# Performance work log

Measured on AMD Instinct MI355X. Metric: run time of the kernel, lower is better.

## Reference

```python
import jax, jax.numpy as jnp
import numpy as np

EPS = 1e-12  # torch F.normalize eps

def _l2n(x, axis):
    n = jnp.linalg.norm(x, axis=axis, keepdims=True)
    return x / jnp.maximum(n, EPS)

def setup_inputs() -> dict:
    key = jax.random.key(0)
    ks = jax.random.split(key, 11)
    B, N, D = 8, 4096, 512
    s = 1.0 / np.sqrt(D)
    return {
        'a': jax.random.normal(ks[0], (B, N, D), jnp.float32),
        'b': jax.random.normal(ks[1], (B, N, D), jnp.float32),
        'Wq': jax.random.normal(ks[2], (D, D), jnp.float32) * s,
        'bq': jax.random.normal(ks[3], (D,), jnp.float32) * s,
        'Wk': jax.random.normal(ks[4], (D, D), jnp.float32) * s,
        'bk': jax.random.normal(ks[5], (D,), jnp.float32) * s,
        'w_g': jax.random.normal(ks[6], (D, 1), jnp.float32),
        'Wp': jax.random.normal(ks[7], (D, D), jnp.float32) * s,
        'bp': jax.random.normal(ks[8], (D,), jnp.float32) * s,
        'Wf': jax.random.normal(ks[9], (D, D), jnp.float32) * s,
        'bf': jax.random.normal(ks[10], (D,), jnp.float32) * s,
    }

def reference(a, b, Wq, bq, Wk, bk, w_g, Wp, bp, Wf, bf):
    D = a.shape[-1]
    scale = D ** (-0.5)
    query = _l2n(jnp.einsum('bnd,ed->bne', a, Wq) + bq, axis=-1)   # [B,N,D]
    key = _l2n(jnp.einsum('bnd,ed->bne', b, Wk) + bk, axis=-1)     # [B,N,D]
    A = (query @ w_g) * scale                                      # [B,N,1]
    A = _l2n(A, axis=1)                                            # normalize over seq
    G = jnp.sum(A * query, axis=1)                                 # [B,D] learned pooling
    gk = G[:, None, :] * key                                       # broadcast [B,N,D]
    out = jnp.einsum('bnd,ed->bne', gk, Wp) + bp + query           # residual
    out = jnp.einsum('bnd,ed->bne', out, Wf) + bf
    return out
```

## Files before the change

### kernel.cpp

```cpp
#include <hip/hip_runtime.h>
#include <stdint.h>

#define DD 512
#define MTOT 32768

typedef float f32x4 __attribute__((ext_vector_type(4)));
typedef __bf16 bf16x8 __attribute__((ext_vector_type(8)));

__device__ __forceinline__ unsigned short f2bf(float f) {
  union { float f; unsigned int u; } c; c.f = f;
  unsigned int r = c.u + 0x7fffu + ((c.u >> 16) & 1u);
  return (unsigned short)(r >> 16);
}
__device__ __forceinline__ float bf2f(unsigned short h) {
  union { unsigned int u; float f; } c; c.u = ((unsigned int)h) << 16;
  return c.f;
}

union FragU { uint4 u; bf16x8 b; };

__global__ __launch_bounds__(256) void convw_k(const float* __restrict__ Wq,
    const float* __restrict__ Wk, const float* __restrict__ Wp,
    const float* __restrict__ Wf, unsigned short* __restrict__ out) {
  int i = (blockIdx.x * 256 + threadIdx.x) * 4;
  int slab = i >> 18;
  int off = i & 262143;
  const float* src = slab == 0 ? Wq : slab == 1 ? Wk : slab == 2 ? Wp : Wf;
  float4 f = *(const float4*)(src + off);
  ushort4 h;
  h.x = f2bf(f.x); h.y = f2bf(f.y); h.z = f2bf(f.z); h.w = f2bf(f.w);
  *(ushort4*)(out + i) = h;
}

template<int AMODE, int EMODE>
__global__ __launch_bounds__(256) void gemm_k(const void* __restrict__ Xv,
    const unsigned short* __restrict__ W, const float* __restrict__ bias,
    const float* __restrict__ Gm, const unsigned short* __restrict__ Qadd,
    void* __restrict__ Cv) {
  constexpr int BM = 128, BK = 32, LDA = 40;
  __shared__ unsigned short As[BM * LDA];
  __shared__ unsigned short Bs[BM * LDA];
  const int tid = threadIdx.x;
  const int lane = tid & 63, wave = tid >> 6;
  const int wr = (wave >> 1) * 64, wc = (wave & 1) * 64;
  const int row0 = blockIdx.x * BM;
  const int col0 = blockIdx.y * BM;
  const int srow = tid >> 1;
  const int skk = (tid & 1) * 16;
  const int fr = lane & 15, quad = lane >> 4;

  f32x4 acc[4][4] = {};

  const float* Gb = nullptr;
  if (AMODE == 2) Gb = Gm + (size_t)(row0 >> 12) * DD;

  for (int k0 = 0; k0 < DD; k0 += BK) {
    unsigned short* adst = &As[srow * LDA + skk];
    if (AMODE == 0) {
      const float* Xr = (const float*)Xv + (size_t)(row0 + srow) * DD + k0 + skk;
#pragma unroll
      for (int q = 0; q < 4; q++) {
        float4 f = ((const float4*)Xr)[q];
        ushort4 h; h.x = f2bf(f.x); h.y = f2bf(f.y); h.z = f2bf(f.z); h.w = f2bf(f.w);
        *(ushort4*)(adst + q * 4) = h;
      }
    } else if (AMODE == 1) {
      const uint4* Xr = (const uint4*)((const unsigned short*)Xv +
                                       (size_t)(row0 + srow) * DD + k0 + skk);
      *(uint4*)adst = Xr[0];
      *(uint4*)(adst + 8) = Xr[1];
    } else {
      const unsigned short* Xr = (const unsigned short*)Xv +
                                 (size_t)(row0 + srow) * DD + k0 + skk;
      const float* Gk = Gb + k0 + skk;
#pragma unroll
      for (int q = 0; q < 4; q++) {
        ushort4 x = *(const ushort4*)(Xr + q * 4);
        float4 g = ((const float4*)Gk)[q];
        ushort4 h;
        h.x = f2bf(bf2f(x.x) * g.x);
        h.y = f2bf(bf2f(x.y) * g.y);
        h.z = f2bf(bf2f(x.z) * g.z);
        h.w = f2bf(bf2f(x.w) * g.w);
        *(ushort4*)(adst + q * 4) = h;
      }
    }
    {
      const uint4* Wr = (const uint4*)(W + (size_t)(col0 + srow) * DD + k0 + skk);
      unsigned short* bdst = &Bs[srow * LDA + skk];
      *(uint4*)bdst = Wr[0];
      *(uint4*)(bdst + 8) = Wr[1];
    }
    __syncthreads();
    bf16x8 af[4], bfr[4];
#pragma unroll
    for (int i = 0; i < 4; i++) {
      FragU u; u.u = *(const uint4*)&As[(wr + i * 16 + fr) * LDA + quad * 8];
      af[i] = u.b;
    }
#pragma unroll
    for (int j = 0; j < 4; j++) {
      FragU u; u.u = *(const uint4*)&Bs[(wc + j * 16 + fr) * LDA + quad * 8];
      bfr[j] = u.b;
    }
#pragma unroll
    for (int i = 0; i < 4; i++)
#pragma unroll
      for (int j = 0; j < 4; j++)
        acc[i][j] = __builtin_amdgcn_mfma_f32_16x16x32_bf16(af[i], bfr[j], acc[i][j], 0, 0, 0);
    __syncthreads();
  }
#pragma unroll
  for (int j = 0; j < 4; j++) {
    int gc = col0 + wc + j * 16 + fr;
    float bv = bias[gc];
#pragma unroll
    for (int i = 0; i < 4; i++) {
      int gr0 = row0 + wr + i * 16 + quad * 4;
#pragma unroll
      for (int r = 0; r < 4; r++) {
        size_t idx = (size_t)(gr0 + r) * DD + gc;
        float v = acc[i][j][r] + bv;
        if (EMODE == 1) v += bf2f(Qadd[idx]);
        if (EMODE <= 1) ((unsigned short*)Cv)[idx] = f2bf(v);
        else            ((float*)Cv)[idx] = v;
      }
    }
  }
}

__global__ __launch_bounds__(256) void norm_k(unsigned short* __restrict__ Q,
    unsigned short* __restrict__ K, const float* __restrict__ wg,
    float* __restrict__ Araw) {
  const int lane = threadIdx.x & 63, wave = threadIdx.x >> 6;
  const size_t row = (size_t)blockIdx.x * 4 + wave;
  unsigned short* p = (blockIdx.y == 0 ? Q : K) + row * DD + lane * 8;
  uint4 u = *(uint4*)p;
  unsigned short* hp = (unsigned short*)&u;
  float v[8];
  float ss = 0.f;
#pragma unroll
  for (int t = 0; t < 8; t++) { v[t] = bf2f(hp[t]); ss += v[t] * v[t]; }
#pragma unroll
  for (int m = 1; m < 64; m <<= 1) ss += __shfl_xor(ss, m, 64);
  float inv = 1.0f / fmaxf(sqrtf(ss), 1e-12f);
#pragma unroll
  for (int t = 0; t < 8; t++) { v[t] *= inv; hp[t] = f2bf(v[t]); }
  *(uint4*)p = u;
  if (blockIdx.y == 0) {
    const float4* wp = (const float4*)(wg + lane * 8);
    float4 w0 = wp[0], w1 = wp[1];
    float dot = v[0] * w0.x + v[1] * w0.y + v[2] * w0.z + v[3] * w0.w +
                v[4] * w1.x + v[5] * w1.y + v[6] * w1.z + v[7] * w1.w;
#pragma unroll
    for (int m = 1; m < 64; m <<= 1) dot += __shfl_xor(dot, m, 64);
    if (lane == 0) Araw[row] = dot;
  }
}

__global__ __launch_bounds__(512) void reduce_s_k(const float* __restrict__ Araw,
    float* __restrict__ sinv, float* __restrict__ G) {
  const int b = blockIdx.x, t = threadIdx.x;
  G[b * DD + t] = 0.f;
  float ss = 0.f;
  for (int i = t; i < 4096; i += 512) { float v = Araw[b * 4096 + i]; ss += v * v; }
#pragma unroll
  for (int m = 1; m < 64; m <<= 1) ss += __shfl_xor(ss, m, 64);
  __shared__ float sred[8];
  if ((t & 63) == 0) sred[t >> 6] = ss;
  __syncthreads();
  if (t == 0) {
    float tot = 0.f;
    for (int i = 0; i < 8; i++) tot += sred[i];
    sinv[b] = 1.0f / fmaxf(sqrtf(tot), 1e-12f);
  }
}

__global__ __launch_bounds__(256) void pool_k(const float* __restrict__ Araw,
    const float* __restrict__ sinv, const unsigned short* __restrict__ Q,
    float* __restrict__ G) {
  const int b = blockIdx.x >> 5;
  const int chunk = blockIdx.x & 31;
  const int rbase = b * 4096 + chunk * 128;
  const float si = sinv[b];
  const int t = threadIdx.x;
  float a0 = 0.f, a1 = 0.f;
  for (int r = 0; r < 128; r++) {
    float w = Araw[rbase + r] * si;
    const unsigned short* qr = Q + (size_t)(rbase + r) * DD;
    a0 += w * bf2f(qr[t]);
    a1 += w * bf2f(qr[t + 256]);
  }
  atomicAdd(&G[b * DD + t], a0);
  atomicAdd(&G[b * DD + t + 256], a1);
}

extern "C" void kernel_launch(void* const* d_in, const int* in_sizes, int n_in,
                              void* d_out, int out_size, void* d_ws, size_t ws_size,
                              hipStream_t stream) {
  const float* a   = (const float*)d_in[0];
  const float* b   = (const float*)d_in[1];
  const float* Wq  = (const float*)d_in[2];
  const float* bq  = (const float*)d_in[3];
  const float* Wk  = (const float*)d_in[4];
  const float* bk  = (const float*)d_in[5];
  const float* wg  = (const float*)d_in[6];
  const float* Wp  = (const float*)d_in[7];
  const float* bp  = (const float*)d_in[8];
  const float* Wf  = (const float*)d_in[9];
  const float* bfb = (const float*)d_in[10];

  char* ws = (char*)d_ws;
  const size_t WELEM = 262144;
  const size_t MD = (size_t)MTOT * DD;
  unsigned short* Wqb = (unsigned short*)ws;
  unsigned short* Wkb = Wqb + WELEM;
  unsigned short* Wpb = Wkb + WELEM;
  unsigned short* Wfb = Wpb + WELEM;
  unsigned short* Qb  = (unsigned short*)(ws + (size_t)2097152);
  unsigned short* Kb  = Qb + MD;
  unsigned short* O1b = Kb + MD;
  float* Araw = (float*)(ws + (size_t)2097152 + 3 * MD * 2);
  float* sinv = Araw + MTOT;
  float* G    = sinv + 64;

  convw_k<<<dim3(1024), dim3(256), 0, stream>>>(Wq, Wk, Wp, Wf, Wqb);
  gemm_k<0, 0><<<dim3(MTOT / 128, 4), dim3(256), 0, stream>>>(a, Wqb, bq, nullptr, nullptr, Qb);
  gemm_k<0, 0><<<dim3(MTOT / 128, 4), dim3(256), 0, stream>>>(b, Wkb, bk, nullptr, nullptr, Kb);
  norm_k<<<dim3(MTOT / 4, 2), dim3(256), 0, stream>>>(Qb, Kb, wg, Araw);
  reduce_s_k<<<dim3(8), dim3(512), 0, stream>>>(Araw, sinv, G);
  pool_k<<<dim3(256), dim3(256), 0, stream>>>(Araw, sinv, Qb, G);
  gemm_k<2, 1><<<dim3(MTOT / 128, 4), dim3(256), 0, stream>>>(Kb, Wpb, bp, G, Qb, O1b);
  gemm_k<1, 2><<<dim3(MTOT / 128, 4), dim3(256), 0, stream>>>(O1b, Wfb, bfb, nullptr, nullptr, d_out);
}
```

Measured before the change: 358.6 us.

## Use direct global-to-LDS loads with swizzled BK=64 tiles and fold G into weights

```diff
diff --git a/kernel.cpp b/kernel.cpp
--- a/kernel.cpp
+++ b/kernel.cpp
@@ -7,107 +7,115 @@
 typedef float f32x4 __attribute__((ext_vector_type(4)));
 typedef __bf16 bf16x8 __attribute__((ext_vector_type(8)));
 
-__device__ __forceinline__ unsigned short f2bf(float f) {
+static __device__ __forceinline__ unsigned short f2bf(float f) {
   union { float f; unsigned int u; } c; c.f = f;
   unsigned int r = c.u + 0x7fffu + ((c.u >> 16) & 1u);
   return (unsigned short)(r >> 16);
 }
-__device__ __forceinline__ float bf2f(unsigned short h) {
+static __device__ __forceinline__ float bf2f(unsigned short h) {
   union { unsigned int u; float f; } c; c.u = ((unsigned int)h) << 16;
   return c.f;
 }
 
 union FragU { uint4 u; bf16x8 b; };
 
-__global__ __launch_bounds__(256) void convw_k(const float* __restrict__ Wq,
-    const float* __restrict__ Wk, const float* __restrict__ Wp,
-    const float* __restrict__ Wf, unsigned short* __restrict__ out) {
+static __device__ __forceinline__ void load_lds16(const void* g, void* l) {
+  __builtin_amdgcn_global_load_lds(
+      (const __attribute__((address_space(1))) void*)g,
+      (__attribute__((address_space(3))) void*)l, 16, 0, 0);
+}
+
+__global__ __launch_bounds__(256) void cvt_k(const float* __restrict__ src,
+                                             unsigned short* __restrict__ dst) {
   int i = (blockIdx.x * 256 + threadIdx.x) * 4;
-  int slab = i >> 18;
-  int off = i & 262143;
-  const float* src = slab == 0 ? Wq : slab == 1 ? Wk : slab == 2 ? Wp : Wf;
-  float4 f = *(const float4*)(src + off);
+  float4 f = *(const float4*)(src + i);
   ushort4 h;
   h.x = f2bf(f.x); h.y = f2bf(f.y); h.z = f2bf(f.z); h.w = f2bf(f.w);
+  *(ushort4*)(dst + i) = h;
+}
+
+__global__ __launch_bounds__(256) void cvt3w_k(const float* __restrict__ W0,
+    const float* __restrict__ W1, const float* __restrict__ W2,
+    unsigned short* __restrict__ D0, unsigned short* __restrict__ D1,
+    unsigned short* __restrict__ D2) {
+  int slab = blockIdx.x >> 8;
+  int off = ((blockIdx.x & 255) * 256 + threadIdx.x) * 4;
+  const float* s = slab == 0 ? W0 : slab == 1 ? W1 : W2;
+  unsigned short* d = slab == 0 ? D0 : slab == 1 ? D1 : D2;
+  float4 f = *(const float4*)(s + off);
+  ushort4 h;
+  h.x = f2bf(f.x); h.y = f2bf(f.y); h.z = f2bf(f.z); h.w = f2bf(f.w);
+  *(ushort4*)(d + off) = h;
+}
+
+__global__ __launch_bounds__(256) void scalew_k(const float* __restrict__ Wp,
+    const float* __restrict__ G, unsigned short* __restrict__ out) {
+  int i = (blockIdx.x * 256 + threadIdx.x) * 4;
+  int b = i >> 18;
+  int rem = i & 262143;
+  int d = rem & 511;
+  float4 w = *(const float4*)(Wp + rem);
+  float4 g = *(const float4*)(G + b * DD + d);
+  ushort4 h;
+  h.x = f2bf(w.x * g.x); h.y = f2bf(w.y * g.y);
+  h.z = f2bf(w.z * g.z); h.w = f2bf(w.w * g.w);
   *(ushort4*)(out + i) = h;
 }
 
-template<int AMODE, int EMODE>
-__global__ __launch_bounds__(256) void gemm_k(const void* __restrict__ Xv,
-    const unsigned short* __restrict__ W, const float* __restrict__ bias,
-    const float* __restrict__ Gm, const unsigned short* __restrict__ Qadd,
+template<int BBATCH, int EMODE>
+__global__ __launch_bounds__(256) void gemm_k(
+    const unsigned short* __restrict__ X,
+    const unsigned short* __restrict__ Wb,
+    const float* __restrict__ bias,
+    const unsigned short* __restrict__ Qadd,
     void* __restrict__ Cv) {
-  constexpr int BM = 128, BK = 32, LDA = 40;
-  __shared__ unsigned short As[BM * LDA];
-  __shared__ unsigned short Bs[BM * LDA];
+  __shared__ unsigned short As[128 * 64];
+  __shared__ unsigned short Bs[128 * 64];
   const int tid = threadIdx.x;
   const int lane = tid & 63, wave = tid >> 6;
+  const int row0 = blockIdx.x * 128, col0 = blockIdx.y * 128;
+  const unsigned short* W = Wb + (BBATCH ? (size_t)(row0 >> 12) * 262144 : 0);
+
+  const int sr = lane >> 3;
+  const int scol = ((lane & 7) ^ sr) * 8;
+  const unsigned short* Ag = X + (size_t)(row0 + wave * 32 + sr) * DD + scol;
+  const unsigned short* Bg = W + (size_t)(col0 + wave * 32 + sr) * DD + scol;
+  const int ldsb = wave * 32 * 64;
+
+  const int fr = lane & 15, quad = lane >> 4;
   const int wr = (wave >> 1) * 64, wc = (wave & 1) * 64;
-  const int row0 = blockIdx.x * BM;
-  const int col0 = blockIdx.y * BM;
-  const int srow = tid >> 1;
-  const int skk = (tid & 1) * 16;
-  const int fr = lane & 15, quad = lane >> 4;
+  const int sw0 = ((quad ^ (fr & 7)) * 8);
+  const int sw1 = (((quad + 4) ^ (fr & 7)) * 8);
 
   f32x4 acc[4][4] = {};
 
-  const float* Gb = nullptr;
-  if (AMODE == 2) Gb = Gm + (size_t)(row0 >> 12) * DD;
-
-  for (int k0 = 0; k0 < DD; k0 += BK) {
-    unsigned short* adst = &As[srow * LDA + skk];
-    if (AMODE == 0) {
-      const float* Xr = (const float*)Xv + (size_t)(row0 + srow) * DD + k0 + skk;
-#pragma unroll
-      for (int q = 0; q < 4; q++) {
-        float4 f = ((const float4*)Xr)[q];
-        ushort4 h; h.x = f2bf(f.x); h.y = f2bf(f.y); h.z = f2bf(f.z); h.w = f2bf(f.w);
-        *(ushort4*)(adst + q * 4) = h;
-      }
-    } else if (AMODE == 1) {
-      const uint4* Xr = (const uint4*)((const unsigned short*)Xv +
-                                       (size_t)(row0 + srow) * DD + k0 + skk);
-      *(uint4*)adst = Xr[0];
-      *(uint4*)(adst + 8) = Xr[1];
-    } else {
-      const unsigned short* Xr = (const unsigned short*)Xv +
-                                 (size_t)(row0 + srow) * DD + k0 + skk;
-      const float* Gk = Gb + k0 + skk;
-#pragma unroll
-      for (int q = 0; q < 4; q++) {
-        ushort4 x = *(const ushort4*)(Xr + q * 4);
-        float4 g = ((const float4*)Gk)[q];
-        ushort4 h;
-        h.x = f2bf(bf2f(x.x) * g.x);
-        h.y = f2bf(bf2f(x.y) * g.y);
-        h.z = f2bf(bf2f(x.z) * g.z);
-        h.w = f2bf(bf2f(x.w) * g.w);
-        *(ushort4*)(adst + q * 4) = h;
-      }
-    }
-    {
-      const uint4* Wr = (const uint4*)(W + (size_t)(col0 + srow) * DD + k0 + skk);
-      unsigned short* bdst = &Bs[srow * LDA + skk];
-      *(uint4*)bdst = Wr[0];
-      *(uint4*)(bdst + 8) = Wr[1];
+  for (int k0 = 0; k0 < DD; k0 += 64) {
+#pragma unroll
+    for (int q = 0; q < 4; q++) {
+      load_lds16(Ag + (size_t)q * 8 * DD + k0, As + ldsb + q * 8 * 64);
+      load_lds16(Bg + (size_t)q * 8 * DD + k0, Bs + ldsb + q * 8 * 64);
     }
     __syncthreads();
-    bf16x8 af[4], bfr[4];
-#pragma unroll
-    for (int i = 0; i < 4; i++) {
-      FragU u; u.u = *(const uint4*)&As[(wr + i * 16 + fr) * LDA + quad * 8];
-      af[i] = u.b;
+#pragma unroll
+    for (int kk = 0; kk < 2; kk++) {
+      const int sw = kk ? sw1 : sw0;
+      bf16x8 af[4], bfr[4];
+#pragma unroll
+      for (int i = 0; i < 4; i++) {
+        FragU u; u.u = *(const uint4*)&As[(wr + i * 16 + fr) * 64 + sw];
+        af[i] = u.b;
+      }
+#pragma unroll
+      for (int j = 0; j < 4; j++) {
+        FragU u; u.u = *(const uint4*)&Bs[(wc + j * 16 + fr) * 64 + sw];
+        bfr[j] = u.b;
+      }
+#pragma unroll
+      for (int i = 0; i < 4; i++)
+#pragma unroll
+        for (int j = 0; j < 4; j++)
+          acc[i][j] = __builtin_amdgcn_mfma_f32_16x16x32_bf16(af[i], bfr[j], acc[i][j], 0, 0, 0);
     }
-#pragma unroll
-    for (int j = 0; j < 4; j++) {
-      FragU u; u.u = *(const uint4*)&Bs[(wc + j * 16 + fr) * LDA + quad * 8];
-      bfr[j] = u.b;
-    }
-#pragma unroll
-    for (int i = 0; i < 4; i++)
-#pragma unroll
-      for (int j = 0; j < 4; j++)
-        acc[i][j] = __builtin_amdgcn_mfma_f32_16x16x32_bf16(af[i], bfr[j], acc[i][j], 0, 0, 0);
     __syncthreads();
   }
 #pragma unroll
@@ -210,26 +218,29 @@
   const float* Wf  = (const float*)d_in[9];
   const float* bfb = (const float*)d_in[10];
 
-  char* ws = (char*)d_ws;
   const size_t WELEM = 262144;
   const size_t MD = (size_t)MTOT * DD;
-  unsigned short* Wqb = (unsigned short*)ws;
+
+  unsigned short* ABb = (unsigned short*)d_ws;
+  unsigned short* Qb  = ABb + MD;
+  unsigned short* Kb  = Qb + MD;
+  unsigned short* Wqb = Kb + MD;
   unsigned short* Wkb = Wqb + WELEM;
-  unsigned short* Wpb = Wkb + WELEM;
-  unsigned short* Wfb = Wpb + WELEM;
-  unsigned short* Qb  = (unsigned short*)(ws + (size_t)2097152);
-  unsigned short* Kb  = Qb + MD;
-  unsigned short* O1b = Kb + MD;
-  float* Araw = (float*)(ws + (size_t)2097152 + 3 * MD * 2);
+  unsigned short* Wfb = Wkb + WELEM;
+  unsigned short* Wps = Wfb + WELEM;
+  float* Araw = (float*)(Wps + 8 * WELEM);
   float* sinv = Araw + MTOT;
   float* G    = sinv + 64;
 
-  convw_k<<<dim3(1024), dim3(256), 0, stream>>>(Wq, Wk, Wp, Wf, Wqb);
-  gemm_k<0, 0><<<dim3(MTOT / 128, 4), dim3(256), 0, stream>>>(a, Wqb, bq, nullptr, nullptr, Qb);
-  gemm_k<0, 0><<<dim3(MTOT / 128, 4), dim3(256), 0, stream>>>(b, Wkb, bk, nullptr, nullptr, Kb);
+  cvt_k<<<dim3(16384), dim3(256), 0, stream>>>(a, ABb);
+  cvt3w_k<<<dim3(768), dim3(256), 0, stream>>>(Wq, Wk, Wf, Wqb, Wkb, Wfb);
+  gemm_k<0, 0><<<dim3(256, 4), dim3(256), 0, stream>>>(ABb, Wqb, bq, nullptr, Qb);
+  cvt_k<<<dim3(16384), dim3(256), 0, stream>>>(b, ABb);
+  gemm_k<0, 0><<<dim3(256, 4), dim3(256), 0, stream>>>(ABb, Wkb, bk, nullptr, Kb);
   norm_k<<<dim3(MTOT / 4, 2), dim3(256), 0, stream>>>(Qb, Kb, wg, Araw);
   reduce_s_k<<<dim3(8), dim3(512), 0, stream>>>(Araw, sinv, G);
   pool_k<<<dim3(256), dim3(256), 0, stream>>>(Araw, sinv, Qb, G);
-  gemm_k<2, 1><<<dim3(MTOT / 128, 4), dim3(256), 0, stream>>>(Kb, Wpb, bp, G, Qb, O1b);
-  gemm_k<1, 2><<<dim3(MTOT / 128, 4), dim3(256), 0, stream>>>(O1b, Wfb, bfb, nullptr, nullptr, d_out);
-}
+  scalew_k<<<dim3(2048), dim3(256), 0, stream>>>(Wp, G, Wps);
+  gemm_k<1, 1><<<dim3(256, 4), dim3(256), 0, stream>>>(Kb, Wps, bp, Qb, ABb);
+  gemm_k<0, 2><<<dim3(256, 4), dim3(256), 0, stream>>>(ABb, Wfb, bfb, nullptr, d_out);
+}
```

Result: faster. 330.6 us (-7.8%).
